# Kernel optimization log

Hardware: AMD Instinct MI355X
Metric: run time of the kernel (lower is better)

## Reference

```python
import jax, jax.numpy as jnp
import numpy as np

N, E, D = 50000, 640000, 128
EPS = 1e-5

def _linear(x, w, b):
    return x @ w.T + b

def _batchnorm(x, gamma, beta):
    # torch_geometric BatchNorm (training mode): batch stats over row axis, biased var
    mu = jnp.mean(x, axis=0)
    var = jnp.mean((x - mu) ** 2, axis=0)
    return gamma * (x - mu) * jax.lax.rsqrt(var + EPS) + beta

def setup_inputs() -> dict:
    key = jax.random.key(0)
    ks = jax.random.split(key, 16)
    s = 0.05
    inp = {
        'h_in': jax.random.normal(ks[0], (N, D), jnp.float32),
        'e_in': jax.random.normal(ks[1], (E, D), jnp.float32),
        'edge_index': jax.random.randint(ks[2], (2, E), 0, N, jnp.int64),
    }
    for i, name in enumerate(['U', 'V', 'A', 'B', 'C']):
        inp[name + '_w'] = jax.random.normal(ks[3 + 2 * i], (D, D), jnp.float32) * s
        inp[name + '_b'] = jax.random.normal(ks[4 + 2 * i], (D,), jnp.float32) * s
    inp['h_gamma'] = jnp.ones((D,), jnp.float32)
    inp['h_beta'] = jnp.zeros((D,), jnp.float32)
    inp['e_gamma'] = jnp.ones((D,), jnp.float32)
    inp['e_beta'] = jnp.zeros((D,), jnp.float32)
    return inp

def reference(h_in, e_in, edge_index, U_w, U_b, V_w, V_b, A_w, A_b, B_w, B_b, C_w, C_b,
              h_gamma, h_beta, e_gamma, e_beta):
    dst, src = edge_index[0], edge_index[1]
    Uh = _linear(h_in, U_w, U_b)           # [N,D]
    Vh = _linear(h_in, V_w, V_b)           # [N,D]
    Ae = _linear(e_in, A_w, A_b)           # [E,D]
    Bh = _linear(h_in, B_w, B_b)           # [N,D]
    Ch = _linear(h_in, C_w, C_b)           # [N,D]
    sigmoid_e = jax.nn.sigmoid(e_in)       # edge_gates=True
    msgs = sigmoid_e * Vh[src]             # [E,D] gather + gate
    agg = jax.ops.segment_sum(msgs, dst, num_segments=N)  # global_add_pool
    h = h_in + jax.nn.relu(_batchnorm(Uh + agg, h_gamma, h_beta))
    e = e_in + jax.nn.relu(_batchnorm(Ae + Bh[dst] + Ch[src], e_gamma, e_beta))
    return (h, e)
```

## Files before the change

kernel.cpp:

```cpp
#include <hip/hip_runtime.h>
#include <math.h>

#define D 128
#define TILE 64
#define PADX 132

typedef __attribute__((ext_vector_type(8))) short s16x8;
typedef __attribute__((ext_vector_type(4))) float f32x4;

__device__ inline ushort f32_to_bf16(float x) {
    unsigned u = __float_as_uint(x);
    return (ushort)((u + 0x7fff + ((u >> 16) & 1)) >> 16);
}
__device__ inline float bf16_to_f32(ushort h) {
    return __uint_as_float(((unsigned)h) << 16);
}

__global__ void zero_misc_k(float* stats, int* deg, int n) {
    int i = blockIdx.x * blockDim.x + threadIdx.x;
    if (i < 512) stats[i] = 0.f;
    if (i < n) deg[i] = 0;
}

__global__ void wconv_k(const float* __restrict__ W, ushort* __restrict__ Wh,
                        ushort* __restrict__ Wl, int n) {
    int i = blockIdx.x * blockDim.x + threadIdx.x;
    if (i < n) {
        float x = W[i];
        ushort h = f32_to_bf16(x);
        Wh[i] = h;
        Wl[i] = f32_to_bf16(x - bf16_to_f32(h));
    }
}

__global__ __launch_bounds__(256, 2)
void node_linear_k(const float* __restrict__ h_in,
                   const float* __restrict__ Uw, const float* __restrict__ Ub,
                   const float* __restrict__ Vw, const float* __restrict__ Vb,
                   const float* __restrict__ Bw, const float* __restrict__ Bb,
                   const float* __restrict__ Cw, const float* __restrict__ Cb,
                   float* __restrict__ outU, float* __restrict__ outV,
                   float* __restrict__ outB, float* __restrict__ outC,
                   int M)
{
    __shared__ float xs[TILE * PADX];
    __shared__ float wsm[D * 68];
    const int tid = threadIdx.x;
    const int row0 = blockIdx.x * TILE;

    for (int f = tid; f < TILE * D / 4; f += 256) {
        int r = f >> 5, c4 = f & 31;
        int row = row0 + r;
        float4 v = make_float4(0.f, 0.f, 0.f, 0.f);
        if (row < M) v = *reinterpret_cast<const float4*>(h_in + (size_t)row * D + c4 * 4);
        *reinterpret_cast<float4*>(&xs[r * PADX + c4 * 4]) = v;
    }

    const int tx = tid & 31;
    const int ty = tid >> 5;

    const float* Ws[4] = {Uw, Vw, Bw, Cw};
    const float* Bs[4] = {Ub, Vb, Bb, Cb};
    float*       Os[4] = {outU, outV, outB, outC};

    #pragma unroll
    for (int wsel = 0; wsel < 4; ++wsel) {
        float acc[8][4];
        #pragma unroll
        for (int r = 0; r < 8; ++r)
            #pragma unroll
            for (int j = 0; j < 4; ++j) acc[r][j] = 0.f;

        const float* W = Ws[wsel];
        #pragma unroll
        for (int half = 0; half < 2; ++half) {
            __syncthreads();
            for (int f = tid; f < D * 64 / 4; f += 256) {
                int j = f >> 4, k4 = f & 15;
                float4 v = *reinterpret_cast<const float4*>(W + (size_t)j * D + half * 64 + k4 * 4);
                *reinterpret_cast<float4*>(&wsm[j * 68 + k4 * 4]) = v;
            }
            __syncthreads();
            #pragma unroll 4
            for (int k4 = 0; k4 < 16; ++k4) {
                float4 wv[4];
                #pragma unroll
                for (int jj = 0; jj < 4; ++jj)
                    wv[jj] = *reinterpret_cast<const float4*>(&wsm[(tx + 32 * jj) * 68 + k4 * 4]);
                #pragma unroll
                for (int r = 0; r < 8; ++r) {
                    float4 av = *reinterpret_cast<const float4*>(&xs[(ty * 8 + r) * PADX + half * 64 + k4 * 4]);
                    #pragma unroll
                    for (int jj = 0; jj < 4; ++jj)
                        acc[r][jj] += av.x * wv[jj].x + av.y * wv[jj].y + av.z * wv[jj].z + av.w * wv[jj].w;
                }
            }
        }
        const float* bias = Bs[wsel];
        float* O = Os[wsel];
        float bv[4];
        #pragma unroll
        for (int jj = 0; jj < 4; ++jj) bv[jj] = bias[tx + 32 * jj];
        #pragma unroll
        for (int r = 0; r < 8; ++r) {
            int row = row0 + ty * 8 + r;
            if (row < M) {
                #pragma unroll
                for (int jj = 0; jj < 4; ++jj)
                    O[(size_t)row * D + tx + 32 * jj] = acc[r][jj] + bv[jj];
            }
        }
    }
}

__global__ void hist_k(const int* __restrict__ dst, int* __restrict__ deg, int E) {
    for (int e = blockIdx.x * blockDim.x + threadIdx.x; e < E; e += gridDim.x * blockDim.x)
        atomicAdd(&deg[dst[e]], 1);
}

__global__ void scan_k(const int* __restrict__ deg, int* __restrict__ off,
                       int* __restrict__ cursor, int n)
{
    __shared__ int wsum[16], wpre[16];
    const int tid = threadIdx.x, lane = tid & 63, w = tid >> 6;
    int carry = 0;
    for (int base = 0; base < n; base += 1024) {
        int i = base + tid;
        int v = (i < n) ? deg[i] : 0;
        int x = v;
        #pragma unroll
        for (int d = 1; d < 64; d <<= 1) {
            int t = __shfl_up(x, d);
            if (lane >= d) x += t;
        }
        if (lane == 63) wsum[w] = x;
        __syncthreads();
        if (tid == 0) {
            int run = carry;
            #pragma unroll
            for (int j = 0; j < 16; ++j) { int t = wsum[j]; wpre[j] = run; run += t; }
            carry = run;
        }
        __syncthreads();
        int excl = wpre[w] + x - v;
        if (i < n) { off[i] = excl; cursor[i] = excl; }
    }
    if (tid == 0) off[n] = carry;
}

__global__ void scatter_k(const int* __restrict__ dst, int* __restrict__ cursor,
                          int* __restrict__ perm, int E)
{
    for (int e = blockIdx.x * blockDim.x + threadIdx.x; e < E; e += gridDim.x * blockDim.x) {
        int pos = atomicAdd(&cursor[dst[e]], 1);
        perm[pos] = e;
    }
}

__global__ __launch_bounds__(256, 3)
void edge_k(const float* __restrict__ e_in,
            const int* __restrict__ eidx,
            const int* __restrict__ perm,
            const ushort* __restrict__ Awh, const ushort* __restrict__ Awl,
            const float* __restrict__ Ab,
            const float* __restrict__ Vh, const float* __restrict__ Bh,
            const float* __restrict__ Ch,
            float* __restrict__ out_h, float* __restrict__ out_e,
            float* __restrict__ e_sum, float* __restrict__ e_sq,
            int E)
{
    __shared__ float xs[TILE * PADX];
    __shared__ ushort bhd[D * 32];
    __shared__ ushort bld[D * 32];
    __shared__ int eids[TILE], dns[TILE], sns[TILE];

    const int tid = threadIdx.x;
    const int w = tid >> 6;
    const int l = tid & 63;
    const int l15 = l & 15;
    const int lk = l >> 4;
    const int e0 = blockIdx.x * TILE;

    if (tid < TILE) {
        int e = e0 + tid;
        int ec = e < E ? e : E - 1;
        int eid = perm[ec];
        eids[tid] = eid;
        dns[tid] = eidx[eid];
        sns[tid] = eidx[(size_t)E + eid];
    }
    __syncthreads();

    for (int f = tid; f < TILE * D / 4; f += 256) {
        int r = f >> 5, c4 = f & 31;
        *reinterpret_cast<float4*>(&xs[r * PADX + c4 * 4]) =
            *reinterpret_cast<const float4*>(e_in + (size_t)eids[r] * D + c4 * 4);
    }
    for (int f = tid; f < 512; f += 256) {
        int row = f >> 2, q = f & 3;
        int c = (q ^ (row & 3)) << 3;
        *reinterpret_cast<s16x8*>(&bhd[row * 32 + c]) =
            *reinterpret_cast<const s16x8*>(Awh + row * D + q * 8);
        *reinterpret_cast<s16x8*>(&bld[row * 32 + c]) =
            *reinterpret_cast<const s16x8*>(Awl + row * D + q * 8);
    }
    __syncthreads();

    s16x8 ahs[4], als[4];
    {
        const int arow = w * 16 + l15;
        #pragma unroll
        for (int s = 0; s < 4; ++s) {
            f32x4 x0 = *reinterpret_cast<const f32x4*>(&xs[arow * PADX + s * 32 + lk * 8]);
            f32x4 x1 = *reinterpret_cast<const f32x4*>(&xs[arow * PADX + s * 32 + lk * 8 + 4]);
            s16x8 h, lo;
            #pragma unroll
            for (int j = 0; j < 4; ++j) {
                ushort hb = f32_to_bf16(x0[j]);
                h[j] = (short)hb;
                lo[j] = (short)f32_to_bf16(x0[j] - bf16_to_f32(hb));
                ushort hb2 = f32_to_bf16(x1[j]);
                h[j + 4] = (short)hb2;
                lo[j + 4] = (short)f32_to_bf16(x1[j] - bf16_to_f32(hb2));
            }
            ahs[s] = h; als[s] = lo;
        }
    }

    f32x4 acc[8];
    #pragma unroll
    for (int n = 0; n < 8; ++n) acc[n] = (f32x4){0.f, 0.f, 0.f, 0.f};

    #pragma unroll
    for (int s = 0; s < 4; ++s) {
        #pragma unroll
        for (int half = 0; half < 2; ++half) {
            s16x8 bh4[4], bl4[4];
            #pragma unroll
            for (int t = 0; t < 4; ++t) {
                int row = (half * 4 + t) * 16 + l15;
                int c = (lk ^ (row & 3)) << 3;
                bh4[t] = *reinterpret_cast<const s16x8*>(&bhd[row * 32 + c]);
                bl4[t] = *reinterpret_cast<const s16x8*>(&bld[row * 32 + c]);
            }
            #pragma unroll
            for (int t = 0; t < 4; ++t) {
                int n = half * 4 + t;
                acc[n] = __builtin_amdgcn_mfma_f32_16x16x32_bf16(ahs[s], bh4[t], acc[n], 0, 0, 0);
                acc[n] = __builtin_amdgcn_mfma_f32_16x16x32_bf16(ahs[s], bl4[t], acc[n], 0, 0, 0);
                acc[n] = __builtin_amdgcn_mfma_f32_16x16x32_bf16(als[s], bh4[t], acc[n], 0, 0, 0);
            }
        }
        __syncthreads();
        if (s < 3) {
            for (int f = tid; f < 512; f += 256) {
                int row = f >> 2, q = f & 3;
                int c = (q ^ (row & 3)) << 3;
                *reinterpret_cast<s16x8*>(&bhd[row * 32 + c]) =
                    *reinterpret_cast<const s16x8*>(Awh + row * D + (s + 1) * 32 + q * 8);
                *reinterpret_cast<s16x8*>(&bld[row * 32 + c]) =
                    *reinterpret_cast<const s16x8*>(Awl + row * D + (s + 1) * 32 + q * 8);
            }
            __syncthreads();
        }
    }

    float abv[8];
    #pragma unroll
    for (int n = 0; n < 8; ++n) abv[n] = Ab[n * 16 + l15];

    float sst[8], sq[8], rs[8];
    #pragma unroll
    for (int n = 0; n < 8; ++n) { sst[n] = 0.f; sq[n] = 0.f; rs[n] = 0.f; }

    const int mrow0 = w * 16 + lk * 4;
    #pragma unroll
    for (int r = 0; r < 4; ++r) {
        int row = mrow0 + r;
        int eid = eids[row], dn = dns[row], sn = sns[row];
        bool valid = (e0 + row) < E;
        if (valid) {
            const float* br = Bh + (size_t)dn * D;
            const float* cr = Ch + (size_t)sn * D;
            float* oe = out_e + (size_t)eid * D;
            #pragma unroll
            for (int n = 0; n < 8; ++n) {
                int col = n * 16 + l15;
                float pre = acc[n][r] + abv[n] + br[col] + cr[col];
                oe[col] = pre;
                sst[n] += pre;
                sq[n] += pre * pre;
            }
        }
        const float* vr = Vh + (size_t)sn * D;
        #pragma unroll
        for (int n = 0; n < 8; ++n) {
            int col = n * 16 + l15;
            float m = valid ? vr[col] / (1.f + __expf(-xs[row * PADX + col])) : 0.f;
            rs[n] += m;
        }
        bool flush = (r == 3) || (dns[row + 1] != dn);
        if (flush) {
            float* dst = out_h + (size_t)dn * D;
            #pragma unroll
            for (int n = 0; n < 8; ++n) {
                unsafeAtomicAdd(dst + n * 16 + l15, rs[n]);
                rs[n] = 0.f;
            }
        }
    }

    #pragma unroll
    for (int n = 0; n < 8; ++n) {
        sst[n] += __shfl_xor(sst[n], 16); sst[n] += __shfl_xor(sst[n], 32);
        sq[n]  += __shfl_xor(sq[n], 16);  sq[n]  += __shfl_xor(sq[n], 32);
    }
    float* sbuf = reinterpret_cast<float*>(bhd);
    float* qbuf = reinterpret_cast<float*>(bld);
    if (l < 16) {
        #pragma unroll
        for (int n = 0; n < 8; ++n) {
            sbuf[w * 128 + n * 16 + l] = sst[n];
            qbuf[w * 128 + n * 16 + l] = sq[n];
        }
    }
    __syncthreads();
    if (tid < 128) {
        float ss = sbuf[tid] + sbuf[128 + tid] + sbuf[256 + tid] + sbuf[384 + tid];
        float qq = qbuf[tid] + qbuf[128 + tid] + qbuf[256 + tid] + qbuf[384 + tid];
        unsafeAtomicAdd(&e_sum[tid], ss);
        unsafeAtomicAdd(&e_sq[tid], qq);
    }
}

__global__ void col_stats_k(const float* __restrict__ X, int rows,
                            float* __restrict__ sum, float* __restrict__ sumsq)
{
    __shared__ float sr[8][128], qr[8][128];
    const int tx = threadIdx.x & 31;
    const int rp = threadIdx.x >> 5;
    float4 s = make_float4(0.f, 0.f, 0.f, 0.f);
    float4 q = make_float4(0.f, 0.f, 0.f, 0.f);
    for (int r = blockIdx.x * 8 + rp; r < rows; r += gridDim.x * 8) {
        float4 v = *reinterpret_cast<const float4*>(X + (size_t)r * D + 4 * tx);
        s.x += v.x; q.x += v.x * v.x;
        s.y += v.y; q.y += v.y * v.y;
        s.z += v.z; q.z += v.z * v.z;
        s.w += v.w; q.w += v.w * v.w;
    }
    *reinterpret_cast<float4*>(&sr[rp][4 * tx]) = s;
    *reinterpret_cast<float4*>(&qr[rp][4 * tx]) = q;
    __syncthreads();
    if (threadIdx.x < 128) {
        float ss = 0.f, qq = 0.f;
        #pragma unroll
        for (int t = 0; t < 8; ++t) { ss += sr[t][threadIdx.x]; qq += qr[t][threadIdx.x]; }
        unsafeAtomicAdd(&sum[threadIdx.x], ss);
        unsafeAtomicAdd(&sumsq[threadIdx.x], qq);
    }
}

__global__ void finalize_k(const float* __restrict__ res_in,
                           float* __restrict__ out,
                           const float* __restrict__ sum, const float* __restrict__ sumsq,
                           const float* __restrict__ gamma, const float* __restrict__ beta,
                           float cntInv, int rows)
{
    const int tx = threadIdx.x & 31;
    const int rp = threadIdx.x >> 5;
    const int col4 = 4 * tx;
    float mu[4], g[4], b[4];
    #pragma unroll
    for (int i = 0; i < 4; ++i) {
        float m = sum[col4 + i] * cntInv;
        float var = sumsq[col4 + i] * cntInv - m * m;
        mu[i] = m;
        g[i] = gamma[col4 + i] * rsqrtf(var + 1e-5f);
        b[i] = beta[col4 + i];
    }
    for (int r = blockIdx.x * 8 + rp; r < rows; r += gridDim.x * 8) {
        size_t o = (size_t)r * D + col4;
        float4 x = *reinterpret_cast<const float4*>(out + o);
        float4 rr = *reinterpret_cast<const float4*>(res_in + o);
        float4 y;
        y.x = rr.x + fmaxf(g[0] * (x.x - mu[0]) + b[0], 0.f);
        y.y = rr.y + fmaxf(g[1] * (x.y - mu[1]) + b[1], 0.f);
        y.z = rr.z + fmaxf(g[2] * (x.z - mu[2]) + b[2], 0.f);
        y.w = rr.w + fmaxf(g[3] * (x.w - mu[3]) + b[3], 0.f);
        *reinterpret_cast<float4*>(out + o) = y;
    }
}

extern "C" void kernel_launch(void* const* d_in, const int* in_sizes, int n_in,
                              void* d_out, int out_size, void* d_ws, size_t ws_size,
                              hipStream_t stream)
{
    const float* h_in = (const float*)d_in[0];
    const float* e_in = (const float*)d_in[1];
    const int*   eidx = (const int*)d_in[2];
    const float* Uw = (const float*)d_in[3];  const float* Ub = (const float*)d_in[4];
    const float* Vw = (const float*)d_in[5];  const float* Vb = (const float*)d_in[6];
    const float* Aw = (const float*)d_in[7];  const float* Ab = (const float*)d_in[8];
    const float* Bw = (const float*)d_in[9];  const float* Bb = (const float*)d_in[10];
    const float* Cw = (const float*)d_in[11]; const float* Cb = (const float*)d_in[12];
    const float* hg = (const float*)d_in[13]; const float* hb = (const float*)d_in[14];
    const float* eg = (const float*)d_in[15]; const float* eb = (const float*)d_in[16];

    const int N = in_sizes[0] / D;
    const int E = in_sizes[1] / D;

    float* out_h = (float*)d_out;
    float* out_e = out_h + (size_t)N * D;

    float* ws = (float*)d_ws;
    float* Vh = ws;
    float* Bh = Vh + (size_t)N * D;
    float* Ch = Bh + (size_t)N * D;
    float* stats = Ch + (size_t)N * D;
    float* h_sum = stats;       float* h_sq = stats + 128;
    float* e_sum = stats + 256; float* e_sq = stats + 384;
    int* deg    = (int*)(stats + 512);
    int* off    = deg + N;
    int* cursor = off + N + 1;
    int* perm   = cursor + N;
    ushort* Awh = (ushort*)(perm + E);
    ushort* Awl = Awh + D * D;

    zero_misc_k<<<(N + 255) / 256, 256, 0, stream>>>(stats, deg, N);
    wconv_k<<<64, 256, 0, stream>>>(Aw, Awh, Awl, D * D);
    hist_k<<<1024, 256, 0, stream>>>(eidx, deg, E);
    scan_k<<<1, 1024, 0, stream>>>(deg, off, cursor, N);
    scatter_k<<<1024, 256, 0, stream>>>(eidx, cursor, perm, E);
    node_linear_k<<<(N + TILE - 1) / TILE, 256, 0, stream>>>(
        h_in, Uw, Ub, Vw, Vb, Bw, Bb, Cw, Cb, out_h, Vh, Bh, Ch, N);
    edge_k<<<(E + TILE - 1) / TILE, 256, 0, stream>>>(
        e_in, eidx, perm, Awh, Awl, Ab, Vh, Bh, Ch, out_h, out_e, e_sum, e_sq, E);
    col_stats_k<<<256, 256, 0, stream>>>(out_h, N, h_sum, h_sq);
    finalize_k<<<256, 256, 0, stream>>>(h_in, out_h, h_sum, h_sq, hg, hb, 1.0f / (float)N, N);
    finalize_k<<<2048, 256, 0, stream>>>(e_in, out_e, e_sum, e_sq, eg, eb, 1.0f / (float)E, E);
}
```

Measured before the change: 1.002 ms.

## Use split-bf16 MFMA for node linears and pre-swizzled fragment weights

Replaces the FP32 SIMT tiled GEMM in the node linear kernel with MFMA 16x16x32 bf16 instructions, using a hi/lo bf16 split (three MFMAs per tile) to keep near-fp32 accuracy. A single weight conversion kernel now pre-swizzles all five weight matrices into per-lane MFMA fragment order in global memory. The edge kernel then reads B fragments straight from global/L2 instead of staging them through LDS with extra barriers, which cuts LDS use and allows higher occupancy. The trade-off is repeated global (L2) weight loads per wave and the cost of split-precision arithmetic.

```diff
diff --git a/kernel.cpp b/kernel.cpp
--- a/kernel.cpp
+++ b/kernel.cpp
@@ -22,92 +22,99 @@
     if (i < n) deg[i] = 0;
 }
 
-__global__ void wconv_k(const float* __restrict__ W, ushort* __restrict__ Wh,
-                        ushort* __restrict__ Wl, int n) {
+__global__ void wconv5_k(const float* __restrict__ W0, const float* __restrict__ W1,
+                         const float* __restrict__ W2, const float* __restrict__ W3,
+                         const float* __restrict__ W4,
+                         ushort* __restrict__ Fh, ushort* __restrict__ Fl) {
     int i = blockIdx.x * blockDim.x + threadIdx.x;
-    if (i < n) {
-        float x = W[i];
-        ushort h = f32_to_bf16(x);
-        Wh[i] = h;
-        Wl[i] = f32_to_bf16(x - bf16_to_f32(h));
-    }
-}
-
-__global__ __launch_bounds__(256, 2)
+    if (i >= 5 * 16384) return;
+    int wsel = i >> 14;
+    int rem = i & 16383;
+    int j = rem & 7;
+    int l = (rem >> 3) & 63;
+    int st = rem >> 9;
+    int s = st >> 3, t = st & 7;
+    int l15 = l & 15, lk = l >> 4;
+    const float* W = wsel == 0 ? W0 : wsel == 1 ? W1 : wsel == 2 ? W2 : wsel == 3 ? W3 : W4;
+    float x = W[(size_t)(t * 16 + l15) * D + s * 32 + lk * 8 + j];
+    ushort h = f32_to_bf16(x);
+    Fh[i] = h;
+    Fl[i] = f32_to_bf16(x - bf16_to_f32(h));
+}
+
+__global__ __launch_bounds__(256, 4)
 void node_linear_k(const float* __restrict__ h_in,
-                   const float* __restrict__ Uw, const float* __restrict__ Ub,
-                   const float* __restrict__ Vw, const float* __restrict__ Vb,
-                   const float* __restrict__ Bw, const float* __restrict__ Bb,
-                   const float* __restrict__ Cw, const float* __restrict__ Cb,
+                   const ushort* __restrict__ Fh, const ushort* __restrict__ Fl,
+                   const float* __restrict__ Ub, const float* __restrict__ Vb,
+                   const float* __restrict__ Bb, const float* __restrict__ Cb,
                    float* __restrict__ outU, float* __restrict__ outV,
                    float* __restrict__ outB, float* __restrict__ outC,
                    int M)
 {
-    __shared__ float xs[TILE * PADX];
-    __shared__ float wsm[D * 68];
     const int tid = threadIdx.x;
+    const int w = tid >> 6, l = tid & 63;
+    const int l15 = l & 15, lk = l >> 4;
     const int row0 = blockIdx.x * TILE;
 
-    for (int f = tid; f < TILE * D / 4; f += 256) {
-        int r = f >> 5, c4 = f & 31;
-        int row = row0 + r;
-        float4 v = make_float4(0.f, 0.f, 0.f, 0.f);
-        if (row < M) v = *reinterpret_cast<const float4*>(h_in + (size_t)row * D + c4 * 4);
-        *reinterpret_cast<float4*>(&xs[r * PADX + c4 * 4]) = v;
-    }
-
-    const int tx = tid & 31;
-    const int ty = tid >> 5;
-
-    const float* Ws[4] = {Uw, Vw, Bw, Cw};
+    s16x8 ahs[4], als[4];
+    {
+        int arow = row0 + w * 16 + l15;
+        if (arow >= M) arow = M - 1;
+        const float* hr = h_in + (size_t)arow * D;
+        #pragma unroll
+        for (int s = 0; s < 4; ++s) {
+            f32x4 x0 = *reinterpret_cast<const f32x4*>(hr + s * 32 + lk * 8);
+            f32x4 x1 = *reinterpret_cast<const f32x4*>(hr + s * 32 + lk * 8 + 4);
+            s16x8 h, lo;
+            #pragma unroll
+            for (int j = 0; j < 4; ++j) {
+                ushort hb = f32_to_bf16(x0[j]);
+                h[j] = (short)hb;
+                lo[j] = (short)f32_to_bf16(x0[j] - bf16_to_f32(hb));
+                ushort hb2 = f32_to_bf16(x1[j]);
+                h[j + 4] = (short)hb2;
+                lo[j + 4] = (short)f32_to_bf16(x1[j] - bf16_to_f32(hb2));
+            }
+            ahs[s] = h; als[s] = lo;
+        }
+    }
+
     const float* Bs[4] = {Ub, Vb, Bb, Cb};
     float*       Os[4] = {outU, outV, outB, outC};
+    const int mrow0 = row0 + w * 16 + lk * 4;
 
     #pragma unroll
     for (int wsel = 0; wsel < 4; ++wsel) {
-        float acc[8][4];
-        #pragma unroll
-        for (int r = 0; r < 8; ++r)
-            #pragma unroll
-            for (int j = 0; j < 4; ++j) acc[r][j] = 0.f;
-
-        const float* W = Ws[wsel];
-        #pragma unroll
-        for (int half = 0; half < 2; ++half) {
-            __syncthreads();
-            for (int f = tid; f < D * 64 / 4; f += 256) {
-                int j = f >> 4, k4 = f & 15;
-                float4 v = *reinterpret_cast<const float4*>(W + (size_t)j * D + half * 64 + k4 * 4);
-                *reinterpret_cast<float4*>(&wsm[j * 68 + k4 * 4]) = v;
-            }
-            __syncthreads();
-            #pragma unroll 4
-            for (int k4 = 0; k4 < 16; ++k4) {
-                float4 wv[4];
-                #pragma unroll
-                for (int jj = 0; jj < 4; ++jj)
-                    wv[jj] = *reinterpret_cast<const float4*>(&wsm[(tx + 32 * jj) * 68 + k4 * 4]);
-                #pragma unroll
-                for (int r = 0; r < 8; ++r) {
-                    float4 av = *reinterpret_cast<const float4*>(&xs[(ty * 8 + r) * PADX + half * 64 + k4 * 4]);
-                    #pragma unroll
-                    for (int jj = 0; jj < 4; ++jj)
-                        acc[r][jj] += av.x * wv[jj].x + av.y * wv[jj].y + av.z * wv[jj].z + av.w * wv[jj].w;
-                }
-            }
-        }
+        f32x4 acc[8];
+        #pragma unroll
+        for (int n = 0; n < 8; ++n) acc[n] = (f32x4){0.f, 0.f, 0.f, 0.f};
+
+        #pragma unroll
+        for (int s = 0; s < 4; ++s) {
+            #pragma unroll
+            for (int t = 0; t < 8; ++t) {
+                size_t fo = ((size_t)((wsel * 32 + s * 8 + t) * 64 + l)) * 8;
+                s16x8 bh = *reinterpret_cast<const s16x8*>(Fh + fo);
+                s16x8 bl = *reinterpret_cast<const s16x8*>(Fl + fo);
+                acc[t] = __builtin_amdgcn_mfma_f32_16x16x32_bf16(ahs[s], bh, acc[t], 0, 0, 0);
+                acc[t] = __builtin_amdgcn_mfma_f32_16x16x32_bf16(ahs[s], bl, acc[t], 0, 0, 0);
+                acc[t] = __builtin_amdgcn_mfma_f32_16x16x32_bf16(als[s], bh, acc[t], 0, 0, 0);
+            }
+        }
+
         const float* bias = Bs[wsel];
         float* O = Os[wsel];
-        float bv[4];
-        #pragma unroll
-        for (int jj = 0; jj < 4; ++jj) bv[jj] = bias[tx + 32 * jj];
-        #pragma unroll
-        for (int r = 0; r < 8; ++r) {
-            int row = row0 + ty * 8 + r;
+        float bv[8];
+        #pragma unroll
+        for (int n = 0; n < 8; ++n) bv[n] = bias[n * 16 + l15];
+        #pragma unroll
+        for (int r = 0; r < 4; ++r) {
+            int row = mrow0 + r;
             if (row < M) {
+                float* orow = O + (size_t)row * D;
                 #pragma unroll
-                for (int jj = 0; jj < 4; ++jj)
-                    O[(size_t)row * D + tx + 32 * jj] = acc[r][jj] + bv[jj];
+                for (int n = 0; n < 8; ++n)
+                    orow[n * 16 + l15] = acc[n][r] + bv[n];
             }
         }
     }
@@ -157,11 +164,11 @@
     }
 }
 
-__global__ __launch_bounds__(256, 3)
+__global__ __launch_bounds__(256, 4)
 void edge_k(const float* __restrict__ e_in,
             const int* __restrict__ eidx,
             const int* __restrict__ perm,
-            const ushort* __restrict__ Awh, const ushort* __restrict__ Awl,
+            const ushort* __restrict__ AFh, const ushort* __restrict__ AFl,
             const float* __restrict__ Ab,
             const float* __restrict__ Vh, const float* __restrict__ Bh,
             const float* __restrict__ Ch,
@@ -170,8 +177,7 @@
             int E)
 {
     __shared__ float xs[TILE * PADX];
-    __shared__ ushort bhd[D * 32];
-    __shared__ ushort bld[D * 32];
+    __shared__ float sbuf[512], qbuf[512];
     __shared__ int eids[TILE], dns[TILE], sns[TILE];
 
     const int tid = threadIdx.x;
@@ -196,14 +202,6 @@
         *reinterpret_cast<float4*>(&xs[r * PADX + c4 * 4]) =
             *reinterpret_cast<const float4*>(e_in + (size_t)eids[r] * D + c4 * 4);
     }
-    for (int f = tid; f < 512; f += 256) {
-        int row = f >> 2, q = f & 3;
-        int c = (q ^ (row & 3)) << 3;
-        *reinterpret_cast<s16x8*>(&bhd[row * 32 + c]) =
-            *reinterpret_cast<const s16x8*>(Awh + row * D + q * 8);
-        *reinterpret_cast<s16x8*>(&bld[row * 32 + c]) =
-            *reinterpret_cast<const s16x8*>(Awl + row * D + q * 8);
-    }
     __syncthreads();
 
     s16x8 ahs[4], als[4];
@@ -234,34 +232,13 @@
     #pragma unroll
     for (int s = 0; s < 4; ++s) {
         #pragma unroll
-        for (int half = 0; half < 2; ++half) {
-            s16x8 bh4[4], bl4[4];
-            #pragma unroll
-            for (int t = 0; t < 4; ++t) {
-                int row = (half * 4 + t) * 16 + l15;
-                int c = (lk ^ (row & 3)) << 3;
-                bh4[t] = *reinterpret_cast<const s16x8*>(&bhd[row * 32 + c]);
-                bl4[t] = *reinterpret_cast<const s16x8*>(&bld[row * 32 + c]);
-            }
-            #pragma unroll
-            for (int t = 0; t < 4; ++t) {
-                int n = half * 4 + t;
-                acc[n] = __builtin_amdgcn_mfma_f32_16x16x32_bf16(ahs[s], bh4[t], acc[n], 0, 0, 0);
-                acc[n] = __builtin_amdgcn_mfma_f32_16x16x32_bf16(ahs[s], bl4[t], acc[n], 0, 0, 0);
-                acc[n] = __builtin_amdgcn_mfma_f32_16x16x32_bf16(als[s], bh4[t], acc[n], 0, 0, 0);
-            }
-        }
-        __syncthreads();
-        if (s < 3) {
-            for (int f = tid; f < 512; f += 256) {
-                int row = f >> 2, q = f & 3;
-                int c = (q ^ (row & 3)) << 3;
-                *reinterpret_cast<s16x8*>(&bhd[row * 32 + c]) =
-                    *reinterpret_cast<const s16x8*>(Awh + row * D + (s + 1) * 32 + q * 8);
-                *reinterpret_cast<s16x8*>(&bld[row * 32 + c]) =
-                    *reinterpret_cast<const s16x8*>(Awl + row * D + (s + 1) * 32 + q * 8);
-            }
-            __syncthreads();
+        for (int t = 0; t < 8; ++t) {
+            size_t fo = ((size_t)((s * 8 + t) * 64 + l)) * 8;
+            s16x8 bh = *reinterpret_cast<const s16x8*>(AFh + fo);
+            s16x8 bl = *reinterpret_cast<const s16x8*>(AFl + fo);
+            acc[t] = __builtin_amdgcn_mfma_f32_16x16x32_bf16(ahs[s], bh, acc[t], 0, 0, 0);
+            acc[t] = __builtin_amdgcn_mfma_f32_16x16x32_bf16(ahs[s], bl, acc[t], 0, 0, 0);
+            acc[t] = __builtin_amdgcn_mfma_f32_16x16x32_bf16(als[s], bh, acc[t], 0, 0, 0);
         }
     }
 
@@ -315,8 +292,6 @@
         sst[n] += __shfl_xor(sst[n], 16); sst[n] += __shfl_xor(sst[n], 32);
         sq[n]  += __shfl_xor(sq[n], 16);  sq[n]  += __shfl_xor(sq[n], 32);
     }
-    float* sbuf = reinterpret_cast<float*>(bhd);
-    float* qbuf = reinterpret_cast<float*>(bld);
     if (l < 16) {
         #pragma unroll
         for (int n = 0; n < 8; ++n) {
@@ -423,18 +398,19 @@
     int* off    = deg + N;
     int* cursor = off + N + 1;
     int* perm   = cursor + N;
-    ushort* Awh = (ushort*)(perm + E);
-    ushort* Awl = Awh + D * D;
+    ushort* Fh = (ushort*)(perm + E);
+    ushort* Fl = Fh + 5 * 16384;
 
     zero_misc_k<<<(N + 255) / 256, 256, 0, stream>>>(stats, deg, N);
-    wconv_k<<<64, 256, 0, stream>>>(Aw, Awh, Awl, D * D);
+    wconv5_k<<<(5 * 16384 + 255) / 256, 256, 0, stream>>>(Uw, Vw, Bw, Cw, Aw, Fh, Fl);
     hist_k<<<1024, 256, 0, stream>>>(eidx, deg, E);
     scan_k<<<1, 1024, 0, stream>>>(deg, off, cursor, N);
     scatter_k<<<1024, 256, 0, stream>>>(eidx, cursor, perm, E);
     node_linear_k<<<(N + TILE - 1) / TILE, 256, 0, stream>>>(
-        h_in, Uw, Ub, Vw, Vb, Bw, Bb, Cw, Cb, out_h, Vh, Bh, Ch, N);
+        h_in, Fh, Fl, Ub, Vb, Bb, Cb, out_h, Vh, Bh, Ch, N);
     edge_k<<<(E + TILE - 1) / TILE, 256, 0, stream>>>(
-        e_in, eidx, perm, Awh, Awl, Ab, Vh, Bh, Ch, out_h, out_e, e_sum, e_sq, E);
+        e_in, eidx, perm, Fh + 4 * 16384, Fl + 4 * 16384, Ab, Vh, Bh, Ch,
+        out_h, out_e, e_sum, e_sq, E);
     col_stats_k<<<256, 256, 0, stream>>>(out_h, N, h_sum, h_sq);
     finalize_k<<<256, 256, 0, stream>>>(h_in, out_h, h_sum, h_sq, hg, hb, 1.0f / (float)N, N);
     finalize_k<<<2048, 256, 0, stream>>>(e_in, out_e, e_sum, e_sq, eg, eb, 1.0f / (float)E, E);
```

New measurement: 877.9 us. 1.14x faster.
